# Kernel optimization log

Hardware: AMD Instinct MI355X
Metric: run time of the kernel (lower is better)

Reference implementation:

```python
import jax, jax.numpy as jnp
import numpy as np

B, T, C, HID, K, H = 8, 1024, 512, 2048, 31, 4  # batch, time, in_chans, hidden_chans, kernel, wshare


def setup_inputs() -> dict:
    key = jax.random.key(0)
    ks = jax.random.split(key, 8)
    n = lambda k_, sh, sc: jax.random.normal(k_, sh, dtype=jnp.float32) * sc
    return {
        "x": n(ks[0], (B, T, C), 1.0),
        "Wl": n(ks[1], (H * K, C), 0.05),      # linear_weight.weight
        "bl": n(ks[2], (H * K,), 0.01),          # linear_weight.bias
        "bias": n(ks[3], (C,), 0.02),            # self.bias
        "Wc": n(ks[4], (HID, C, K), 0.01),       # pointwise_conv1.weight (O,I,K)
        "bc": n(ks[5], (HID,), 0.01),            # pointwise_conv1.bias
        "W2": n(ks[6], (C, HID), 0.01),          # w_2.weight
        "b2": n(ks[7], (C,), 0.01),              # w_2.bias
    }


def reference(x, Wl, bl, bias, Wc, bc, W2, b2):
    Bq, Tq, Cq = x.shape
    d = Cq // H  # channels per weight-share head
    # dynamic conv logits: (B,T,H,K)
    logits = (x @ Wl.T + bl).reshape(Bq, Tq, H, K)
    # banded positions: output t attends to t + j - (K-1)//2
    offs = jnp.arange(K) - (K - 1) // 2
    pos = jnp.arange(Tq)[:, None] + offs[None, :]          # (T,K)
    valid = (pos >= 0) & (pos < Tq)
    logits = jnp.where(valid[None, :, None, :], logits, -jnp.inf)
    w = jax.nn.softmax(logits, axis=-1)                     # softmax over window (matches banded softmax over T)
    # gather windowed inputs: (B,T,K,H,d)
    xg = x.reshape(Bq, Tq, H, d)[:, jnp.clip(pos, 0, Tq - 1)]
    y = jnp.einsum('bthk,btkhd->bthd', w, xg).reshape(Bq, Tq, Cq)
    # (B,C,T) + bias
    y = y.transpose(0, 2, 1) + bias[None, :, None]
    # pointwise_conv1: Conv1d(C->HID, kernel K, padding 0) -> T' = T-K+1
    z = jax.lax.conv_general_dilated(y, Wc, (1,), 'VALID',
                                     dimension_numbers=('NCH', 'OIH', 'NCH'))
    z = z + bc[None, :, None]
    z = jax.nn.selu(z.transpose(0, 2, 1))                   # (B,T',HID)
    return z @ W2.T + b2                                    # (B,T',C)
```

## Files before the change

### kernel.cpp

```cpp
#include <hip/hip_runtime.h>
#include <hip/hip_bf16.h>

typedef __attribute__((ext_vector_type(8))) short short8;
typedef __attribute__((ext_vector_type(4))) float f32x4;

#define NB 8
#define NT 1024
#define NC 512
#define NHID 2048
#define NK 31
#define NH 4
#define NTP 994
#define MROWS (NB * NTP)
#define TG 4

__device__ __forceinline__ void gload_lds16(const void* g, void* l) {
  __builtin_amdgcn_global_load_lds(
      (const __attribute__((address_space(1))) void*)g,
      (__attribute__((address_space(3))) void*)l, 16, 0, 0);
}

#define FENCE() __builtin_amdgcn_sched_barrier(0)
#define SBAR()                                  \
  do {                                          \
    FENCE();                                    \
    __builtin_amdgcn_s_barrier();               \
    FENCE();                                    \
  } while (0)
#define WLGKM(n)                                                 \
  do {                                                           \
    FENCE();                                                     \
    asm volatile("s_waitcnt lgkmcnt(" #n ")" ::: "memory");      \
    FENCE();                                                     \
  } while (0)
#define WVM(n)                                                   \
  do {                                                           \
    FENCE();                                                     \
    asm volatile("s_waitcnt vmcnt(" #n ")" ::: "memory");        \
    FENCE();                                                     \
  } while (0)

__global__ __launch_bounds__(256) void prep_wc(const float* __restrict__ Wc,
                                               __hip_bfloat16* __restrict__ Wt) {
  const int blk = blockIdx.x;
  const int cb = blk & 7;
  const int o0 = (blk >> 3) << 3;
  const int c0 = cb << 6;
  const int obig = o0 >> 8;
  const int orb = o0 & 255;
  __shared__ float lds[8 * 64 * NK];
  for (int ol = 0; ol < 8; ++ol) {
    const float* src = Wc + ((size_t)(o0 + ol) * NC + c0) * NK;
    for (int i = threadIdx.x; i < 64 * NK; i += 256) lds[ol * (64 * NK) + i] = src[i];
  }
  __syncthreads();
  for (int i = threadIdx.x; i < NK * 8 * 64; i += 256) {
    const int k = i >> 9;
    const int rem = i & 511;
    const int ol = rem >> 6;
    const int ci = rem & 63;
    Wt[((size_t)((obig * 8 + cb) * NK + k) << 14) + ((orb + ol) << 6) + (ci ^ (ol << 3))] =
        __float2bfloat16(lds[ol * (64 * NK) + ci * NK + k]);
  }
}

__global__ __launch_bounds__(256) void prep_w2(const float* __restrict__ W2,
                                               __hip_bfloat16* __restrict__ W2t) {
  const int i = blockIdx.x * 256 + threadIdx.x;
  if (i < 32 * 512 * 64) {
    const int oi = i & 63;
    const int c = (i >> 6) & 511;
    const int kb = i >> 15;
    const size_t dst = ((size_t)(((c >> 7) * 32 + kb) * 128 + (c & 127)) << 6) +
                       (oi ^ ((c & 7) << 3));
    W2t[dst] = __float2bfloat16(W2[(size_t)c * NHID + (kb << 6) + oi]);
  }
}

__global__ __launch_bounds__(256) void dynconv(const float* __restrict__ x,
                                               const float* __restrict__ Wl,
                                               const float* __restrict__ bl,
                                               const float* __restrict__ bias,
                                               __hip_bfloat16* __restrict__ Y) {
  const int t0 = blockIdx.x * TG;
  const int b = blockIdx.y;
  const int tid = threadIdx.x, lane = tid & 63, w = tid >> 6;
  __shared__ float xt[TG][NC];
  __shared__ float lg[TG][NH * NK];
  __shared__ float wsm[TG][NH][NK];

  for (int i = tid; i < TG * NC; i += 256) {
    const int tg = i >> 9, c = i & 511;
    xt[tg][c] = x[((size_t)b * NT + t0 + tg) * NC + c];
  }
  __syncthreads();

  for (int i = 0; i < 31; ++i) {
    const int id = (i << 2) | w;
    const float* wrow = Wl + (size_t)id * NC + (lane << 3);
    float wv[8];
#pragma unroll
    for (int u = 0; u < 8; ++u) wv[u] = wrow[u];
    const float blv = bl[id];
#pragma unroll
    for (int tg = 0; tg < TG; ++tg) {
      float s = 0.f;
#pragma unroll
      for (int u = 0; u < 8; ++u) s += xt[tg][(lane << 3) + u] * wv[u];
#pragma unroll
      for (int off = 32; off; off >>= 1) s += __shfl_xor(s, off);
      if (lane == 0) lg[tg][id] = s + blv;
    }
  }
  __syncthreads();

  if (tid < TG * NH) {
    const int tg = tid >> 2, h = tid & 3;
    const int t = t0 + tg;
    int jlo = 15 - t; if (jlo < 0) jlo = 0;
    int jhi = 1038 - t; if (jhi > 30) jhi = 30;
    float mx = -1e30f;
    for (int j = jlo; j <= jhi; ++j) mx = fmaxf(mx, lg[tg][h * NK + j]);
    float ssum = 0.f;
    for (int j = 0; j < NK; ++j) {
      const float e = (j >= jlo && j <= jhi) ? __expf(lg[tg][h * NK + j] - mx) : 0.f;
      wsm[tg][h][j] = e;
      ssum += e;
    }
    const float inv = 1.f / ssum;
    for (int j = 0; j < NK; ++j) wsm[tg][h][j] *= inv;
  }
  __syncthreads();

  const int c = tid << 1;
  const int h = c >> 7;
  const float2* x2 = (const float2*)x;
  const float bias0 = bias[c], bias1 = bias[c + 1];
#pragma unroll
  for (int tg = 0; tg < TG; ++tg) {
    const int t = t0 + tg;
    float a0 = 0.f, a1 = 0.f;
#pragma unroll
    for (int j = 0; j < NK; ++j) {
      int pos = t + j - 15;
      pos = pos < 0 ? 0 : (pos > NT - 1 ? NT - 1 : pos);
      const float wgt = wsm[tg][h][j];
      const float2 v = x2[(((size_t)b * NT + pos) << 8) + tid];
      a0 += wgt * v.x;
      a1 += wgt * v.y;
    }
    const int cs = (c & ~63) | ((c & 63) ^ ((t & 7) << 3));
    __hip_bfloat162 hv;
    hv.x = __float2bfloat16(a0 + bias0);
    hv.y = __float2bfloat16(a1 + bias1);
    *(__hip_bfloat162*)(Y + ((size_t)b * NT + t) * NC + cs) = hv;
  }
}

__global__ __launch_bounds__(512, 2) void conv_gemm(const __hip_bfloat16* __restrict__ Y,
                                                    const __hip_bfloat16* __restrict__ Wt,
                                                    const float* __restrict__ bc,
                                                    __hip_bfloat16* __restrict__ Z) {
  const int o0 = blockIdx.x << 8;
  const int t0 = blockIdx.y << 8;
  const int b = blockIdx.z;
  __shared__ __align__(16) __hip_bfloat16 Ys[288 * 64];
  __shared__ __align__(16) __hip_bfloat16 Bsm[3][256 * 64];
  const int tid = threadIdx.x;
  const int lane = tid & 63, wid = tid >> 6;
  const int wr = wid >> 2, wcid = wid & 3;
  const int obig = o0 >> 8;

  f32x4 acc[8][4] = {};

  auto stageY = [&](int cb_) {
    const int c0 = cb_ << 6;
#pragma unroll
    for (int p = 0; p < 5; ++p) {
      const int i = (p << 9) + tid;
      if (i < 2304) {
        int grow = t0 + (i >> 3);
        if (grow > NT - 1) grow = NT - 1;
        gload_lds16(Y + (((size_t)b * NT + grow) << 9) + c0 + ((i & 7) << 3),
                    &Ys[i << 3]);
      }
    }
  };
  auto stageBc = [&](__hip_bfloat16* dst, int s_, int p) {
    const __hip_bfloat16* wb = Wt + (((size_t)(obig * 248 + s_)) << 14);
    const int i = (p << 9) + tid;
    gload_lds16(wb + (i << 3), dst + (i << 3));
  };

  __hip_bfloat16* b0 = Bsm[0];
  __hip_bfloat16* b1 = Bsm[1];
  __hip_bfloat16* b2 = Bsm[2];

  stageY(0);
#pragma unroll
  for (int p = 0; p < 4; ++p) stageBc(b0, 0, p);
#pragma unroll
  for (int p = 0; p < 4; ++p) stageBc(b1, 1, p);

  const int l15 = lane & 15;
  const int kob = (lane >> 4) << 3;
  const int R0 = (wr << 7) + l15;
  const int bkey = (l15 & 7) << 3;

  int boff[2][2][2];
#pragma unroll
  for (int kk = 0; kk < 2; ++kk)
#pragma unroll
    for (int hf = 0; hf < 2; ++hf)
#pragma unroll
      for (int n = 0; n < 2; ++n) {
        const int br = (wcid << 6) + (hf << 5) + (n << 4) + l15;
        boff[kk][hf][n] = (br << 6) + (((kk << 5) | kob) ^ bkey);
      }

  for (int cb = 0; cb < 8; ++cb) {
    for (int k = 0; k < NK; ++k) {
      const int s = cb * 31 + k;
      const bool st = (s <= 245);

      if ((k == 0 && cb > 0) || s == 247) { WVM(0); } else { WVM(4); }
      SBAR();

      const int keyv = ((l15 + k) & 7) << 3;
      const int ako0 = kob ^ keyv;
      const int ako1 = (32 | kob) ^ keyv;
      const int arow = (R0 + k) << 6;

      short8 av0[4], av1[4], a20[4], a21[4];
      short8 bl0[2], bl1[2], bh0[2], bh1[2];

#pragma unroll
      for (int m = 0; m < 4; ++m) {
        av0[m] = *(const short8*)&Ys[arow + (m << 10) + ako0];
        av1[m] = *(const short8*)&Ys[arow + (m << 10) + ako1];
      }
#pragma unroll
      for (int n = 0; n < 2; ++n) {
        bl0[n] = *(const short8*)&b0[boff[0][0][n]];
        bl1[n] = *(const short8*)&b0[boff[1][0][n]];
        bh0[n] = *(const short8*)&b0[boff[0][1][n]];
        bh1[n] = *(const short8*)&b0[boff[1][1][n]];
      }
      if (st) stageBc(b2, s + 2, 0);

      WLGKM(4);
      __builtin_amdgcn_s_setprio(1);
#pragma unroll
      for (int m = 0; m < 4; ++m)
#pragma unroll
        for (int n = 0; n < 2; ++n)
          acc[m][n] = __builtin_amdgcn_mfma_f32_16x16x32_bf16(av0[m], bl0[n], acc[m][n], 0, 0, 0);
#pragma unroll
      for (int m = 0; m < 4; ++m)
#pragma unroll
        for (int n = 0; n < 2; ++n)
          acc[m][n] = __builtin_amdgcn_mfma_f32_16x16x32_bf16(av1[m], bl1[n], acc[m][n], 0, 0, 0);
      __builtin_amdgcn_s_setprio(0);

      if (st) stageBc(b2, s + 2, 1);
#pragma unroll
      for (int m = 0; m < 4; ++m) {
        a20[m] = *(const short8*)&Ys[arow + 4096 + (m << 10) + ako0];
        a21[m] = *(const short8*)&Ys[arow + 4096 + (m << 10) + ako1];
      }

      WLGKM(8);
      __builtin_amdgcn_s_setprio(1);
#pragma unroll
      for (int m = 0; m < 4; ++m)
#pragma unroll
        for (int n = 0; n < 2; ++n)
          acc[m][2 + n] = __builtin_amdgcn_mfma_f32_16x16x32_bf16(av0[m], bh0[n], acc[m][2 + n], 0, 0, 0);
#pragma unroll
      for (int m = 0; m < 4; ++m)
#pragma unroll
        for (int n = 0; n < 2; ++n)
          acc[m][2 + n] = __builtin_amdgcn_mfma_f32_16x16x32_bf16(av1[m], bh1[n], acc[m][2 + n], 0, 0, 0);
      __builtin_amdgcn_s_setprio(0);

      if (st) stageBc(b2, s + 2, 2);

      WLGKM(0);
      __builtin_amdgcn_s_setprio(1);
#pragma unroll
      for (int m = 0; m < 4; ++m)
#pragma unroll
        for (int n = 0; n < 2; ++n)
          acc[4 + m][2 + n] = __builtin_amdgcn_mfma_f32_16x16x32_bf16(a20[m], bh0[n], acc[4 + m][2 + n], 0, 0, 0);
#pragma unroll
      for (int m = 0; m < 4; ++m)
#pragma unroll
        for (int n = 0; n < 2; ++n)
          acc[4 + m][2 + n] = __builtin_amdgcn_mfma_f32_16x16x32_bf16(a21[m], bh1[n], acc[4 + m][2 + n], 0, 0, 0);
#pragma unroll
      for (int m = 0; m < 4; ++m)
#pragma unroll
        for (int n = 0; n < 2; ++n)
          acc[4 + m][n] = __builtin_amdgcn_mfma_f32_16x16x32_bf16(a20[m], bl0[n], acc[4 + m][n], 0, 0, 0);
#pragma unroll
      for (int m = 0; m < 4; ++m)
#pragma unroll
        for (int n = 0; n < 2; ++n)
          acc[4 + m][n] = __builtin_amdgcn_mfma_f32_16x16x32_bf16(a21[m], bl1[n], acc[4 + m][n], 0, 0, 0);
      __builtin_amdgcn_s_setprio(0);

      if (st) stageBc(b2, s + 2, 3);

      __hip_bfloat16* tp = b0; b0 = b1; b1 = b2; b2 = tp;
    }
    if (cb < 7) {
      SBAR();
      stageY(cb + 1);
    }
  }

  const float kS = 1.0507009873554805f;
  const float kAS = 1.7580993408473766f;
#pragma unroll
  for (int n = 0; n < 4; ++n) {
    const int col = o0 + (wcid << 6) + (n << 4) + (lane & 15);
    const float bcv = bc[col];
#pragma unroll
    for (int m = 0; m < 8; ++m) {
      const int rbase = (wr << 7) + (m << 4) + ((lane >> 4) << 2);
#pragma unroll
      for (int r = 0; r < 4; ++r) {
        const int tp = t0 + rbase + r;
        if (tp < NTP) {
          const float v = acc[m][n][r] + bcv;
          const float s = v > 0.f ? kS * v : kAS * (__expf(v) - 1.f);
          const size_t grow = (size_t)b * NTP + tp;
          const int cs = (col & ~63) | ((col & 63) ^ (((int)(grow & 7)) << 3));
          Z[grow * NHID + cs] = __float2bfloat16(s);
        }
      }
    }
  }
}

__global__ __launch_bounds__(256) void out_gemm(const __hip_bfloat16* __restrict__ Zm,
                                                const __hip_bfloat16* __restrict__ W2t,
                                                const float* __restrict__ b2,
                                                float* __restrict__ Out) {
  const int n0 = blockIdx.x << 7;
  const int m0 = blockIdx.y << 7;
  __shared__ __align__(16) __hip_bfloat16 As[128 * 64];
  __shared__ __align__(16) __hip_bfloat16 Bs[128 * 64];
  const int tid = threadIdx.x;
  const int lane = tid & 63, wid = tid >> 6;
  const int wr = wid >> 1, wc = wid & 1;

  f32x4 acc[4][4] = {};

  for (int kb = 0; kb < 32; ++kb) {
#pragma unroll
    for (int p = 0; p < 4; ++p) {
      const int i = (p << 8) + tid;
      int row = m0 + (i >> 3);
      if (row > MROWS - 1) row = MROWS - 1;
      gload_lds16(Zm + ((size_t)row << 11) + (kb << 6) + ((i & 7) << 3), &As[i << 3]);
    }
    const __hip_bfloat16* wb = W2t + ((size_t)((n0 >> 7) * 32 + kb) << 13);
#pragma unroll
    for (int p = 0; p < 4; ++p) {
      const int i = (p << 8) + tid;
      gload_lds16(wb + (i << 3), &Bs[i << 3]);
    }
    __syncthreads();
#pragma unroll
    for (int kk = 0; kk < 2; ++kk) {
      const int ko = (kk << 5) + ((lane >> 4) << 3);
      short8 av[4], bv[4];
#pragma unroll
      for (int m = 0; m < 4; ++m) {
        const int r = (wr << 6) + (m << 4) + (lane & 15);
        av[m] = *(const short8*)&As[(r << 6) + (ko ^ ((r & 7) << 3))];
      }
#pragma unroll
      for (int n = 0; n < 4; ++n) {
        const int br = (wc << 6) + (n << 4) + (lane & 15);
        bv[n] = *(const short8*)&Bs[(br << 6) + (ko ^ ((br & 7) << 3))];
      }
#pragma unroll
      for (int m = 0; m < 4; ++m)
#pragma unroll
        for (int n = 0; n < 4; ++n)
          acc[m][n] = __builtin_amdgcn_mfma_f32_16x16x32_bf16(av[m], bv[n], acc[m][n], 0, 0, 0);
    }
    __syncthreads();
  }

#pragma unroll
  for (int n = 0; n < 4; ++n) {
    const int col = n0 + (wc << 6) + (n << 4) + (lane & 15);
    const float b2v = b2[col];
#pragma unroll
    for (int m = 0; m < 4; ++m) {
      const int rbase = m0 + (wr << 6) + (m << 4) + ((lane >> 4) << 2);
#pragma unroll
      for (int r = 0; r < 4; ++r) {
        const int row = rbase + r;
        if (row < MROWS) Out[(size_t)row * NC + col] = acc[m][n][r] + b2v;
      }
    }
  }
}

extern "C" void kernel_launch(void* const* d_in, const int* in_sizes, int n_in,
                              void* d_out, int out_size, void* d_ws, size_t ws_size,
                              hipStream_t stream) {
  const float* x = (const float*)d_in[0];
  const float* Wl = (const float*)d_in[1];
  const float* bl = (const float*)d_in[2];
  const float* bias = (const float*)d_in[3];
  const float* Wc = (const float*)d_in[4];
  const float* bc = (const float*)d_in[5];
  const float* W2 = (const float*)d_in[6];
  const float* b2 = (const float*)d_in[7];
  float* out = (float*)d_out;

  char* ws = (char*)d_ws;
  __hip_bfloat16* Wt = (__hip_bfloat16*)(ws);
  __hip_bfloat16* Y = (__hip_bfloat16*)(ws + 65011712);
  __hip_bfloat16* W2t = (__hip_bfloat16*)(ws + 73400320);
  __hip_bfloat16* Z = (__hip_bfloat16*)(ws + 75497472);

  hipLaunchKernelGGL(prep_wc, dim3(2048), dim3(256), 0, stream, Wc, Wt);
  hipLaunchKernelGGL(prep_w2, dim3(4096), dim3(256), 0, stream, W2, W2t);
  hipLaunchKernelGGL(dynconv, dim3(NT / TG, NB), dim3(256), 0, stream, x, Wl, bl, bias, Y);
  hipLaunchKernelGGL(conv_gemm, dim3(NHID / 256, 4, NB), dim3(512), 0, stream, Y, Wt, bc, Z);
  hipLaunchKernelGGL(out_gemm, dim3(NC / 128, (MROWS + 127) / 128), dim3(256), 0, stream,
                     Z, W2t, b2, out);
}
```

Measured before the change: 645.2 us.

## Vectorize dynconv loads, stage conv_gemm epilogue via LDS, double-buffer out_gemm

```diff
diff --git a/kernel.cpp b/kernel.cpp
--- a/kernel.cpp
+++ b/kernel.cpp
@@ -2,6 +2,7 @@
 #include <hip/hip_bf16.h>
 
 typedef __attribute__((ext_vector_type(8))) short short8;
+typedef __attribute__((ext_vector_type(4))) short short4v;
 typedef __attribute__((ext_vector_type(4))) float f32x4;
 
 #define NB 8
@@ -89,11 +90,19 @@
   __shared__ float lg[TG][NH * NK];
   __shared__ float wsm[TG][NH][NK];
 
-  for (int i = tid; i < TG * NC; i += 256) {
-    const int tg = i >> 9, c = i & 511;
-    xt[tg][c] = x[((size_t)b * NT + t0 + tg) * NC + c];
+  {
+    const float4* xsrc = (const float4*)(x + ((size_t)b * NT + t0) * NC);
+    float4* xdst = (float4*)xt;
+#pragma unroll
+    for (int i = 0; i < 2; ++i) xdst[(i << 8) + tid] = xsrc[(i << 8) + tid];
   }
   __syncthreads();
+
+  float xv[TG][8];
+#pragma unroll
+  for (int tg = 0; tg < TG; ++tg)
+#pragma unroll
+    for (int u = 0; u < 8; ++u) xv[tg][u] = xt[tg][(lane << 3) + u];
 
   for (int i = 0; i < 31; ++i) {
     const int id = (i << 2) | w;
@@ -106,7 +115,7 @@
     for (int tg = 0; tg < TG; ++tg) {
       float s = 0.f;
 #pragma unroll
-      for (int u = 0; u < 8; ++u) s += xt[tg][(lane << 3) + u] * wv[u];
+      for (int u = 0; u < 8; ++u) s += xv[tg][u] * wv[u];
 #pragma unroll
       for (int off = 32; off; off >>= 1) s += __shfl_xor(s, off);
       if (lane == 0) lg[tg][id] = s + blv;
@@ -132,28 +141,30 @@
   }
   __syncthreads();
 
-  const int c = tid << 1;
-  const int h = c >> 7;
-  const float2* x2 = (const float2*)x;
-  const float bias0 = bias[c], bias1 = bias[c + 1];
-#pragma unroll
-  for (int tg = 0; tg < TG; ++tg) {
+  const int grp = tid >> 7;
+  const int ct = tid & 127;
+  const int c4 = ct << 2;
+  const int h = c4 >> 7;
+  const float4* x4 = (const float4*)x;
+  const float4 b4 = ((const float4*)bias)[ct];
+  for (int tg = grp; tg < TG; tg += 2) {
     const int t = t0 + tg;
-    float a0 = 0.f, a1 = 0.f;
+    float a0 = 0.f, a1 = 0.f, a2 = 0.f, a3 = 0.f;
 #pragma unroll
     for (int j = 0; j < NK; ++j) {
       int pos = t + j - 15;
       pos = pos < 0 ? 0 : (pos > NT - 1 ? NT - 1 : pos);
       const float wgt = wsm[tg][h][j];
-      const float2 v = x2[(((size_t)b * NT + pos) << 8) + tid];
-      a0 += wgt * v.x;
-      a1 += wgt * v.y;
-    }
-    const int cs = (c & ~63) | ((c & 63) ^ ((t & 7) << 3));
-    __hip_bfloat162 hv;
-    hv.x = __float2bfloat16(a0 + bias0);
-    hv.y = __float2bfloat16(a1 + bias1);
-    *(__hip_bfloat162*)(Y + ((size_t)b * NT + t) * NC + cs) = hv;
+      const float4 v = x4[(((size_t)b * NT + pos) << 7) + ct];
+      a0 += wgt * v.x; a1 += wgt * v.y; a2 += wgt * v.z; a3 += wgt * v.w;
+    }
+    const int cs = (c4 & ~63) | ((c4 & 63) ^ ((t & 7) << 3));
+    union { short4v s4; __hip_bfloat16 hh[4]; } u;
+    u.hh[0] = __float2bfloat16(a0 + b4.x);
+    u.hh[1] = __float2bfloat16(a1 + b4.y);
+    u.hh[2] = __float2bfloat16(a2 + b4.z);
+    u.hh[3] = __float2bfloat16(a3 + b4.w);
+    *(short4v*)(Y + ((size_t)b * NT + t) * NC + cs) = u.s4;
   }
 }
 
@@ -164,8 +175,11 @@
   const int o0 = blockIdx.x << 8;
   const int t0 = blockIdx.y << 8;
   const int b = blockIdx.z;
-  __shared__ __align__(16) __hip_bfloat16 Ys[288 * 64];
-  __shared__ __align__(16) __hip_bfloat16 Bsm[3][256 * 64];
+  __shared__ __align__(16) char pool[135168];
+  __hip_bfloat16* Ys = (__hip_bfloat16*)pool;
+  __hip_bfloat16* b0 = (__hip_bfloat16*)(pool + 36864);
+  __hip_bfloat16* b1 = (__hip_bfloat16*)(pool + 36864 + 32768);
+  __hip_bfloat16* b2 = (__hip_bfloat16*)(pool + 36864 + 65536);
   const int tid = threadIdx.x;
   const int lane = tid & 63, wid = tid >> 6;
   const int wr = wid >> 2, wcid = wid & 3;
@@ -192,10 +206,6 @@
     gload_lds16(wb + (i << 3), dst + (i << 3));
   };
 
-  __hip_bfloat16* b0 = Bsm[0];
-  __hip_bfloat16* b1 = Bsm[1];
-  __hip_bfloat16* b2 = Bsm[2];
-
   stageY(0);
 #pragma unroll
   for (int p = 0; p < 4; ++p) stageBc(b0, 0, p);
@@ -319,26 +329,36 @@
     }
   }
 
+  SBAR();
+  __hip_bfloat16* zt = (__hip_bfloat16*)pool;
   const float kS = 1.0507009873554805f;
   const float kAS = 1.7580993408473766f;
+  const int l15e = lane & 15;
 #pragma unroll
   for (int n = 0; n < 4; ++n) {
-    const int col = o0 + (wcid << 6) + (n << 4) + (lane & 15);
-    const float bcv = bc[col];
+    const int col = (wcid << 6) + (n << 4) + l15e;
+    const float bcv = bc[o0 + col];
 #pragma unroll
     for (int m = 0; m < 8; ++m) {
-      const int rbase = (wr << 7) + (m << 4) + ((lane >> 4) << 2);
+      const int rb = (wr << 7) + (m << 4) + ((lane >> 4) << 2);
 #pragma unroll
       for (int r = 0; r < 4; ++r) {
-        const int tp = t0 + rbase + r;
-        if (tp < NTP) {
-          const float v = acc[m][n][r] + bcv;
-          const float s = v > 0.f ? kS * v : kAS * (__expf(v) - 1.f);
-          const size_t grow = (size_t)b * NTP + tp;
-          const int cs = (col & ~63) | ((col & 63) ^ (((int)(grow & 7)) << 3));
-          Z[grow * NHID + cs] = __float2bfloat16(s);
-        }
-      }
+        const float v = acc[m][n][r] + bcv;
+        const float sv = v > 0.f ? kS * v : kAS * (__expf(v) - 1.f);
+        zt[(rb + r) * 264 + col] = __float2bfloat16(sv);
+      }
+    }
+  }
+  __syncthreads();
+  for (int j = tid; j < 8192; j += 512) {
+    const int row = j >> 5;
+    const int c8 = (j & 31) << 3;
+    const int tp = t0 + row;
+    if (tp < NTP) {
+      const size_t grow = (size_t)b * NTP + tp;
+      const int key = ((int)grow & 7) << 3;
+      const int cs = (c8 & ~63) | ((c8 & 63) ^ key);
+      *(short8*)(Z + grow * NHID + o0 + cs) = *(const short8*)&zt[row * 264 + c8];
     }
   }
 }
@@ -349,29 +369,36 @@
                                                 float* __restrict__ Out) {
   const int n0 = blockIdx.x << 7;
   const int m0 = blockIdx.y << 7;
-  __shared__ __align__(16) __hip_bfloat16 As[128 * 64];
-  __shared__ __align__(16) __hip_bfloat16 Bs[128 * 64];
+  __shared__ __align__(16) __hip_bfloat16 As[2][128 * 64];
+  __shared__ __align__(16) __hip_bfloat16 Bs[2][128 * 64];
   const int tid = threadIdx.x;
   const int lane = tid & 63, wid = tid >> 6;
   const int wr = wid >> 1, wc = wid & 1;
 
-  f32x4 acc[4][4] = {};
-
-  for (int kb = 0; kb < 32; ++kb) {
+  auto stage = [&](int bufi, int kb_) {
 #pragma unroll
     for (int p = 0; p < 4; ++p) {
       const int i = (p << 8) + tid;
       int row = m0 + (i >> 3);
       if (row > MROWS - 1) row = MROWS - 1;
-      gload_lds16(Zm + ((size_t)row << 11) + (kb << 6) + ((i & 7) << 3), &As[i << 3]);
-    }
-    const __hip_bfloat16* wb = W2t + ((size_t)((n0 >> 7) * 32 + kb) << 13);
+      gload_lds16(Zm + ((size_t)row << 11) + (kb_ << 6) + ((i & 7) << 3),
+                  &As[bufi][i << 3]);
+    }
+    const __hip_bfloat16* wb = W2t + ((size_t)((n0 >> 7) * 32 + kb_) << 13);
 #pragma unroll
     for (int p = 0; p < 4; ++p) {
       const int i = (p << 8) + tid;
-      gload_lds16(wb + (i << 3), &Bs[i << 3]);
-    }
+      gload_lds16(wb + (i << 3), &Bs[bufi][i << 3]);
+    }
+  };
+
+  f32x4 acc[4][4] = {};
+  stage(0, 0);
+
+  for (int kb = 0; kb < 32; ++kb) {
+    const int buf = kb & 1;
     __syncthreads();
+    if (kb < 31) stage(buf ^ 1, kb + 1);
 #pragma unroll
     for (int kk = 0; kk < 2; ++kk) {
       const int ko = (kk << 5) + ((lane >> 4) << 3);
@@ -379,12 +406,12 @@
 #pragma unroll
       for (int m = 0; m < 4; ++m) {
         const int r = (wr << 6) + (m << 4) + (lane & 15);
-        av[m] = *(const short8*)&As[(r << 6) + (ko ^ ((r & 7) << 3))];
+        av[m] = *(const short8*)&As[buf][(r << 6) + (ko ^ ((r & 7) << 3))];
       }
 #pragma unroll
       for (int n = 0; n < 4; ++n) {
         const int br = (wc << 6) + (n << 4) + (lane & 15);
-        bv[n] = *(const short8*)&Bs[(br << 6) + (ko ^ ((br & 7) << 3))];
+        bv[n] = *(const short8*)&Bs[buf][(br << 6) + (ko ^ ((br & 7) << 3))];
       }
 #pragma unroll
       for (int m = 0; m < 4; ++m)
@@ -392,7 +419,6 @@
         for (int n = 0; n < 4; ++n)
           acc[m][n] = __builtin_amdgcn_mfma_f32_16x16x32_bf16(av[m], bv[n], acc[m][n], 0, 0, 0);
     }
-    __syncthreads();
   }
 
 #pragma unroll
```

Measured after the change: 577.2 us, median of 2. 10.5% less time.
